# Kernel tuning notes

Measured on AMD Instinct MI355X. Metric: run time of the kernel, lower is better.

## Reference

```python
import jax, jax.numpy as jnp
import numpy as np

N_HEADS = 16

def setup_inputs() -> dict:
    key = jax.random.key(0)
    k1, k2, k3 = jax.random.split(key, 3)
    B, T, C = 4, 2048, 1024
    x = jax.random.normal(k1, (B, T, C), dtype=jnp.float32)
    w_qkv = jax.random.normal(k2, (C, 3 * C), dtype=jnp.float32) * (1.0 / np.sqrt(C))
    w_out = jax.random.normal(k3, (C, C), dtype=jnp.float32) * (1.0 / np.sqrt(C))
    return {"x": x, "w_qkv": w_qkv, "w_out": w_out}

def reference(x, w_qkv, w_out):
    B, T, C = x.shape
    H = N_HEADS
    D = C // H
    qkv = jnp.einsum('btc,cf->btf', x, w_qkv).reshape(B, T, 3, H, D)
    q, k, v = qkv[:, :, 0], qkv[:, :, 1], qkv[:, :, 2]  # [B,T,H,D]
    q = q.transpose(0, 2, 1, 3)  # [B,H,T,D]
    k = k.transpose(0, 2, 1, 3)
    v = v.transpose(0, 2, 1, 3)
    scale = 1.0 / jnp.sqrt(jnp.asarray(D, dtype=x.dtype))
    scores = jnp.einsum('bhqd,bhkd->bhqk', q, k) * scale  # [B,H,T,T]
    causal = jnp.tril(jnp.ones((T, T), dtype=bool))
    scores = jnp.where(causal[None, None], scores, jnp.asarray(-jnp.inf, dtype=scores.dtype))
    attn = jax.nn.softmax(scores, axis=-1)
    ctx = jnp.einsum('bhqk,bhkd->bhqd', attn, v)  # [B,H,T,D]
    ctx = ctx.transpose(0, 2, 1, 3).reshape(B, T, C)
    return jnp.einsum('btc,co->bto', ctx, w_out)
```

## Files before the change

kernel.cpp:

```cpp
#include <hip/hip_runtime.h>

typedef __attribute__((ext_vector_type(8))) short bf16x8;
typedef __attribute__((ext_vector_type(4))) short bf16x4;
typedef __attribute__((ext_vector_type(4))) float f32x4;
typedef __attribute__((ext_vector_type(4))) unsigned short u16x4;

#define MFMA16(a, b, c) __builtin_amdgcn_mfma_f32_16x16x32_bf16((a), (b), (c), 0, 0, 0)
#define MFMA16K16(a, b, c) __builtin_amdgcn_mfma_f32_16x16x16bf16_1k((a), (b), (c), 0, 0, 0)

__device__ __forceinline__ unsigned short f2bf(float f) {
    union { float f; unsigned int u; } x; x.f = f;
    unsigned int r = x.u + 0x7FFFu + ((x.u >> 16) & 1u);
    return (unsigned short)(r >> 16);
}
__device__ __forceinline__ unsigned int fbits(float f) {
    union { float f; unsigned int u; } x; x.f = f;
    return x.u;
}
__device__ __forceinline__ void gload_lds16(const void* g, void* l) {
    __builtin_amdgcn_global_load_lds(
        (const __attribute__((address_space(1))) unsigned int*)g,
        (__attribute__((address_space(3))) unsigned int*)l,
        16, 0, 0);
}

__global__ void cast_x(const float* __restrict__ in, unsigned short* __restrict__ hi,
                       int n) {
    int i = (blockIdx.x * blockDim.x + threadIdx.x) * 4;
    if (i >= n) return;
    float4 v = *(const float4*)(in + i);
    float vv[4] = {v.x, v.y, v.z, v.w};
    u16x4 h;
#pragma unroll
    for (int j = 0; j < 4; ++j) h[j] = f2bf(vv[j]);
    *(u16x4*)(hi + i) = h;
}

__global__ void tcast_k(const float* __restrict__ in, unsigned short* __restrict__ out,
                        int K, int N) {
    __shared__ float tile[64][65];
    int n0 = blockIdx.x * 64, k0 = blockIdx.y * 64;
    for (int i = threadIdx.x; i < 4096; i += 256) {
        int r = i >> 6, c = i & 63;
        tile[r][c] = in[(size_t)(k0 + r) * N + n0 + c];
    }
    __syncthreads();
    for (int i = threadIdx.x; i < 4096; i += 256) {
        int r = i >> 6, c = i & 63;
        out[(size_t)(n0 + r) * K + k0 + c] = f2bf(tile[c][r]);
    }
}

__global__ __launch_bounds__(256, 2) void gemm_qkv(
    const unsigned short* __restrict__ A,
    const unsigned short* __restrict__ Bt,
    unsigned short* __restrict__ qout, unsigned short* __restrict__ kout,
    unsigned short* __restrict__ vtout) {
    const int K = 1024;
    __shared__ __align__(16) unsigned short sA[128 * 64], sB[128 * 64];
    int tid = threadIdx.x, lane = tid & 63, w = tid >> 6;
    int c = lane & 15, quad = lane >> 4;
    int sw = c & 7;
    int wm = (w >> 1) * 64, wn = (w & 1) * 64;
    int m0 = blockIdx.y * 128, n0 = blockIdx.x * 128;

    f32x4 acc[4][4];
#pragma unroll
    for (int i = 0; i < 4; i++)
#pragma unroll
        for (int j = 0; j < 4; j++) acc[i][j] = (f32x4){0.f, 0.f, 0.f, 0.f};

    for (int kk = 0; kk < K; kk += 64) {
#pragma unroll
        for (int p = 0; p < 4; ++p) {
            int ch = p * 256 + tid;
            int r = ch >> 3;
            int gs = (ch & 7) ^ (r & 7);
            gload_lds16(A + (size_t)(m0 + r) * K + kk + gs * 8, &sA[ch * 8]);
            gload_lds16(Bt + (size_t)(n0 + r) * K + kk + gs * 8, &sB[ch * 8]);
        }
        __syncthreads();
#pragma unroll
        for (int ks8 = 0; ks8 < 8; ks8 += 4) {
            bf16x8 af[4], bfr[4];
#pragma unroll
            for (int mt = 0; mt < 4; ++mt)
                af[mt] = *(const bf16x8*)&sA[(wm + mt * 16 + c) * 64 +
                                             ((ks8 + quad) ^ sw) * 8];
#pragma unroll
            for (int nt = 0; nt < 4; ++nt)
                bfr[nt] = *(const bf16x8*)&sB[(wn + nt * 16 + c) * 64 +
                                              ((ks8 + quad) ^ sw) * 8];
#pragma unroll
            for (int mt = 0; mt < 4; ++mt)
#pragma unroll
                for (int nt = 0; nt < 4; ++nt)
                    acc[mt][nt] = MFMA16(af[mt], bfr[nt], acc[mt][nt]);
        }
        __syncthreads();
    }

    const float QSCALE = 0.1803368801111601f;
#pragma unroll
    for (int mt = 0; mt < 4; ++mt) {
#pragma unroll
        for (int nt = 0; nt < 4; ++nt) {
#pragma unroll
            for (int r = 0; r < 4; ++r) {
                int row = m0 + wm + mt * 16 + quad * 4 + r;
                int col = n0 + wn + nt * 16 + c;
                float v = acc[mt][nt][r];
                int which = col >> 10;
                int h = (col >> 6) & 15;
                int d = col & 63;
                int b = row >> 11;
                int t = row & 2047;
                size_t bh_ = (size_t)(b * 16 + h);
                if (which == 0)
                    qout[(bh_ * 2048 + t) * 64 + d] = f2bf(v * QSCALE);
                else if (which == 1)
                    kout[(bh_ * 2048 + t) * 64 + d] = f2bf(v);
                else
                    vtout[(bh_ * 64 + d) * 2048 + t] = f2bf(v);
            }
        }
    }
}

__global__ __launch_bounds__(256, 2) void gemm2_bt(
    const unsigned short* __restrict__ A,
    const unsigned short* __restrict__ Bt,
    float* __restrict__ out) {
    const int K = 1024, N = 1024;
    __shared__ __align__(16) unsigned short sA[128 * 64], sB[128 * 64];
    int tid = threadIdx.x, lane = tid & 63, w = tid >> 6;
    int c = lane & 15, quad = lane >> 4;
    int sw = c & 7;
    int wm = (w >> 1) * 64, wn = (w & 1) * 64;
    int m0 = blockIdx.y * 128, n0 = blockIdx.x * 128;

    f32x4 acc[4][4];
#pragma unroll
    for (int i = 0; i < 4; i++)
#pragma unroll
        for (int j = 0; j < 4; j++) acc[i][j] = (f32x4){0.f, 0.f, 0.f, 0.f};

    for (int kk = 0; kk < K; kk += 64) {
#pragma unroll
        for (int p = 0; p < 4; ++p) {
            int ch = p * 256 + tid;
            int r = ch >> 3;
            int gs = (ch & 7) ^ (r & 7);
            gload_lds16(A + (size_t)(m0 + r) * K + kk + gs * 8, &sA[ch * 8]);
            gload_lds16(Bt + (size_t)(n0 + r) * K + kk + gs * 8, &sB[ch * 8]);
        }
        __syncthreads();
#pragma unroll
        for (int ks8 = 0; ks8 < 8; ks8 += 4) {
            bf16x8 af[4], bfr[4];
#pragma unroll
            for (int mt = 0; mt < 4; ++mt)
                af[mt] = *(const bf16x8*)&sA[(wm + mt * 16 + c) * 64 +
                                             ((ks8 + quad) ^ sw) * 8];
#pragma unroll
            for (int nt = 0; nt < 4; ++nt)
                bfr[nt] = *(const bf16x8*)&sB[(wn + nt * 16 + c) * 64 +
                                              ((ks8 + quad) ^ sw) * 8];
#pragma unroll
            for (int mt = 0; mt < 4; ++mt)
#pragma unroll
                for (int nt = 0; nt < 4; ++nt)
                    acc[mt][nt] = MFMA16(af[mt], bfr[nt], acc[mt][nt]);
        }
        __syncthreads();
    }

#pragma unroll
    for (int mt = 0; mt < 4; ++mt)
#pragma unroll
        for (int nt = 0; nt < 4; ++nt)
#pragma unroll
            for (int r = 0; r < 4; ++r) {
                int row = m0 + wm + mt * 16 + quad * 4 + r;
                int col = n0 + wn + nt * 16 + c;
                out[(size_t)row * N + col] = acc[mt][nt][r];
            }
}

#define SSTR 72
__global__ __launch_bounds__(256, 4) void attn_k(
    const unsigned short* __restrict__ q,
    const unsigned short* __restrict__ k,
    const unsigned short* __restrict__ vt,
    unsigned short* __restrict__ ctx) {
    const int T = 2048, D = 64;
    __shared__ __align__(16) unsigned short sK[2][64 * SSTR];
    __shared__ __align__(16) unsigned short sV[2][64 * SSTR];

    int tid = threadIdx.x, lane = tid & 63, w = tid >> 6;
    int c = lane & 15, quad = lane >> 4;

    int j = blockIdx.x;
    int g4 = j >> 8, q4 = (j >> 4) & 15, low = j & 15;
    int jt = (g4 & 1) ? q4 : (15 - q4);
    int bh = g4 * 16 + low;
    int b = bh >> 4, hh = bh & 15;

    const unsigned short* qh = q + (size_t)bh * T * D;
    const unsigned short* kh = k + (size_t)bh * T * D;
    const unsigned short* vh = vt + (size_t)bh * D * T;

    int dv = tid >> 3, tcv = (tid & 7) * 8;
    int q0 = jt * 128;
    int nkt = 2 * jt + 2;
    int qloc = w * 16 + c;
    int qrow[2];
    qrow[0] = q0 + qloc;
    qrow[1] = qrow[0] + 64;

    bf16x8 bq[2][2];
#pragma unroll
    for (int g = 0; g < 2; ++g) {
        bq[g][0] = *(const bf16x8*)&qh[(size_t)qrow[g] * D + quad * 8];
        bq[g][1] = *(const bf16x8*)&qh[(size_t)qrow[g] * D + 32 + quad * 8];
    }

    f32x4 o[2][4];
#pragma unroll
    for (int g = 0; g < 2; ++g)
#pragma unroll
        for (int nt = 0; nt < 4; ++nt) o[g][nt] = (f32x4){0.f, 0.f, 0.f, 0.f};
    float l_i[2] = {0.f, 0.f};

    bf16x8 kr0 = *(const bf16x8*)&kh[(size_t)lane * D + w * 8];
    bf16x8 kr1 = *(const bf16x8*)&kh[(size_t)lane * D + w * 8 + 32];
    bf16x8 vr0 = *(const bf16x8*)&vh[(size_t)dv * T + tcv];
    bf16x8 vr1 = *(const bf16x8*)&vh[(size_t)(dv + 32) * T + tcv];
    *(bf16x8*)&sK[0][lane * SSTR + w * 8] = kr0;
    *(bf16x8*)&sK[0][lane * SSTR + w * 8 + 32] = kr1;
    *(bf16x8*)&sV[0][dv * SSTR + tcv] = vr0;
    *(bf16x8*)&sV[0][(dv + 32) * SSTR + tcv] = vr1;
    __syncthreads();

    int cur = 0;
    for (int kt = 0; kt < nkt; ++kt) {
        int kb = kt * 64;
        if (kt + 1 < nkt) {
            int kb2 = kb + 64;
            kr0 = *(const bf16x8*)&kh[(size_t)(kb2 + lane) * D + w * 8];
            kr1 = *(const bf16x8*)&kh[(size_t)(kb2 + lane) * D + w * 8 + 32];
            vr0 = *(const bf16x8*)&vh[(size_t)dv * T + kb2 + tcv];
            vr1 = *(const bf16x8*)&vh[(size_t)(dv + 32) * T + kb2 + tcv];
        }
        bool g0_active = (kt + 1 < nkt);

        const unsigned short* sKc = sK[cur];
        const unsigned short* sVc = sV[cur];

        f32x4 st[2][4];
        __builtin_amdgcn_s_setprio(1);
#pragma unroll
        for (int mt = 0; mt < 4; ++mt) {
            bf16x8 ak0 = *(const bf16x8*)&sKc[(mt * 16 + c) * SSTR + quad * 8];
            bf16x8 ak1 = *(const bf16x8*)&sKc[(mt * 16 + c) * SSTR + 32 + quad * 8];
#pragma unroll
            for (int g = 0; g < 2; ++g) {
                f32x4 z = (f32x4){0.f, 0.f, 0.f, 0.f};
                z = MFMA16(ak0, bq[g][0], z);
                z = MFMA16(ak1, bq[g][1], z);
                st[g][mt] = z;
            }
        }
        __builtin_amdgcn_s_setprio(0);

        bf16x4 pf[2][4];
#pragma unroll
        for (int g = 0; g < 2; ++g) {
            if (g == 0 && !g0_active) continue;
            bool diag = (kb == q0 + (g << 6));
            if (diag) {
#pragma unroll
                for (int mt = 0; mt < 4; ++mt)
#pragma unroll
                    for (int r = 0; r < 4; ++r)
                        if (mt * 16 + quad * 4 + r > qloc) st[g][mt][r] = -1.0e30f;
            }
            float rs = 0.f;
#pragma unroll
            for (int mt = 0; mt < 4; ++mt) {
                float p0 = __builtin_exp2f(st[g][mt][0]);
                float p1 = __builtin_exp2f(st[g][mt][1]);
                float p2 = __builtin_exp2f(st[g][mt][2]);
                float p3 = __builtin_exp2f(st[g][mt][3]);
                rs += (p0 + p1) + (p2 + p3);
                unsigned int w0 = __builtin_amdgcn_perm(
                    fbits(p1) + 0x8000u, fbits(p0) + 0x8000u, 0x07060302u);
                unsigned int w1 = __builtin_amdgcn_perm(
                    fbits(p3) + 0x8000u, fbits(p2) + 0x8000u, 0x07060302u);
                uint2 pk; pk.x = w0; pk.y = w1;
                pf[g][mt] = *(bf16x4*)&pk;
            }
            l_i[g] += rs;
        }

        __builtin_amdgcn_s_setprio(1);
#pragma unroll
        for (int mt = 0; mt < 4; ++mt) {
#pragma unroll
            for (int nt = 0; nt < 4; ++nt) {
                bf16x4 av = *(const bf16x4*)&sVc[(nt * 16 + c) * SSTR + mt * 16 + quad * 4];
                if (g0_active) o[0][nt] = MFMA16K16(av, pf[0][mt], o[0][nt]);
                o[1][nt] = MFMA16K16(av, pf[1][mt], o[1][nt]);
            }
        }
        __builtin_amdgcn_s_setprio(0);

        if (kt + 1 < nkt) {
            int nxt = cur ^ 1;
            *(bf16x8*)&sK[nxt][lane * SSTR + w * 8] = kr0;
            *(bf16x8*)&sK[nxt][lane * SSTR + w * 8 + 32] = kr1;
            *(bf16x8*)&sV[nxt][dv * SSTR + tcv] = vr0;
            *(bf16x8*)&sV[nxt][(dv + 32) * SSTR + tcv] = vr1;
            __syncthreads();
            cur = nxt;
        }
    }

#pragma unroll
    for (int g = 0; g < 2; ++g) {
        float l = l_i[g];
        l += __shfl_xor(l, 16);
        l += __shfl_xor(l, 32);
        float inv = 1.0f / l;
#pragma unroll
        for (int nt = 0; nt < 4; ++nt) {
            u16x4 ob;
#pragma unroll
            for (int r = 0; r < 4; ++r) ob[r] = f2bf(o[g][nt][r] * inv);
            *(u16x4*)&ctx[(size_t)(b * T + qrow[g]) * 1024 + hh * 64 + nt * 16 + quad * 4] = ob;
        }
    }
}

extern "C" void kernel_launch(void* const* d_in, const int* in_sizes, int n_in,
                              void* d_out, int out_size, void* d_ws, size_t ws_size,
                              hipStream_t stream) {
    const float* x     = (const float*)d_in[0];
    const float* w_qkv = (const float*)d_in[1];
    const float* w_out = (const float*)d_in[2];
    float* out = (float*)d_out;

    char* ws = (char*)d_ws;
    unsigned short* wqkvt = (unsigned short*)(ws + 0);
    unsigned short* woutt = (unsigned short*)(ws + 6291456);
    unsigned short* x_bf  = (unsigned short*)(ws + 8388608);
    unsigned short* qb    = (unsigned short*)(ws + 25165824);
    unsigned short* kb    = (unsigned short*)(ws + 41943040);
    unsigned short* vtb   = (unsigned short*)(ws + 58720256);
    unsigned short* ctx   = (unsigned short*)(ws + 8388608);

    cast_x<<<8192, 256, 0, stream>>>(x, x_bf, 8388608);
    tcast_k<<<dim3(48, 16), 256, 0, stream>>>(w_qkv, wqkvt, 1024, 3072);
    tcast_k<<<dim3(16, 16), 256, 0, stream>>>(w_out, woutt, 1024, 1024);
    gemm_qkv<<<dim3(24, 64), 256, 0, stream>>>(x_bf, wqkvt, qb, kb, vtb);
    attn_k<<<1024, 256, 0, stream>>>(qb, kb, vtb, ctx);
    gemm2_bt<<<dim3(8, 64), 256, 0, stream>>>(ctx, woutt, out);
}
```

Before: 266.7 us.

## Split long causal attention rows into two KV halves with atomic merge

Query tiles with long causal KV ranges (jt 8-15) are split into two blocks, each covering half of the KV tiles. Each half accumulates unnormalized partial outputs and row sums into a scratch buffer with float atomics, and a new merge kernel normalizes the result and writes ctx. The output buffer is reused as scratch and zeroed inside the cast kernel. Blocks are issued in a longest-first job order to balance load. The goal is to shorten the tail of the causal workload, at the cost of atomic traffic and an extra kernel launch. The merge is valid only because the softmax skips the max-subtraction.

```diff
diff --git a/kernel.cpp b/kernel.cpp
--- a/kernel.cpp
+++ b/kernel.cpp
@@ -25,15 +25,18 @@
 }
 
 __global__ void cast_x(const float* __restrict__ in, unsigned short* __restrict__ hi,
-                       int n) {
-    int i = (blockIdx.x * blockDim.x + threadIdx.x) * 4;
-    if (i >= n) return;
-    float4 v = *(const float4*)(in + i);
-    float vv[4] = {v.x, v.y, v.z, v.w};
-    u16x4 h;
-#pragma unroll
-    for (int j = 0; j < 4; ++j) h[j] = f2bf(vv[j]);
-    *(u16x4*)(hi + i) = h;
+                       int n, float4* __restrict__ zptr, int zn) {
+    int idx = blockIdx.x * blockDim.x + threadIdx.x;
+    int i = idx * 4;
+    if (i < n) {
+        float4 v = *(const float4*)(in + i);
+        float vv[4] = {v.x, v.y, v.z, v.w};
+        u16x4 h;
+#pragma unroll
+        for (int j = 0; j < 4; ++j) h[j] = f2bf(vv[j]);
+        *(u16x4*)(hi + i) = h;
+    }
+    if (idx < zn) zptr[idx] = (float4){0.f, 0.f, 0.f, 0.f};
 }
 
 __global__ void tcast_k(const float* __restrict__ in, unsigned short* __restrict__ out,
@@ -188,11 +191,15 @@
 }
 
 #define SSTR 72
+__device__ const int JOB_ORDER[24] = {7, 15, 23, 14, 22, 6,  13, 21, 12, 20, 5,  11,
+                                      19, 10, 18, 4,  9,  17, 8,  16, 3,  2,  1,  0};
+
 __global__ __launch_bounds__(256, 4) void attn_k(
     const unsigned short* __restrict__ q,
     const unsigned short* __restrict__ k,
     const unsigned short* __restrict__ vt,
-    unsigned short* __restrict__ ctx) {
+    unsigned short* __restrict__ ctx,
+    float* __restrict__ op, float* __restrict__ lbuf) {
     const int T = 2048, D = 64;
     __shared__ __align__(16) unsigned short sK[2][64 * SSTR];
     __shared__ __align__(16) unsigned short sV[2][64 * SSTR];
@@ -200,10 +207,14 @@
     int tid = threadIdx.x, lane = tid & 63, w = tid >> 6;
     int c = lane & 15, quad = lane >> 4;
 
-    int j = blockIdx.x;
-    int g4 = j >> 8, q4 = (j >> 4) & 15, low = j & 15;
-    int jt = (g4 & 1) ? q4 : (15 - q4);
-    int bh = g4 * 16 + low;
+    int rank = blockIdx.x >> 6, bh = blockIdx.x & 63;
+    int t = JOB_ORDER[rank];
+    int jt, kt0, nkt;
+    bool split, has_diag;
+    if (t < 8)        { jt = t;     kt0 = 0;      nkt = 2 * t + 2; split = false; has_diag = true; }
+    else if (t < 16)  { jt = t;     kt0 = 0;      nkt = jt + 1;    split = true;  has_diag = false; }
+    else              { jt = t - 8; kt0 = jt + 1; nkt = jt + 1;    split = true;  has_diag = true; }
+    int kt_end = kt0 + nkt;
     int b = bh >> 4, hh = bh & 15;
 
     const unsigned short* qh = q + (size_t)bh * T * D;
@@ -212,7 +223,6 @@
 
     int dv = tid >> 3, tcv = (tid & 7) * 8;
     int q0 = jt * 128;
-    int nkt = 2 * jt + 2;
     int qloc = w * 16 + c;
     int qrow[2];
     qrow[0] = q0 + qloc;
@@ -232,10 +242,11 @@
         for (int nt = 0; nt < 4; ++nt) o[g][nt] = (f32x4){0.f, 0.f, 0.f, 0.f};
     float l_i[2] = {0.f, 0.f};
 
-    bf16x8 kr0 = *(const bf16x8*)&kh[(size_t)lane * D + w * 8];
-    bf16x8 kr1 = *(const bf16x8*)&kh[(size_t)lane * D + w * 8 + 32];
-    bf16x8 vr0 = *(const bf16x8*)&vh[(size_t)dv * T + tcv];
-    bf16x8 vr1 = *(const bf16x8*)&vh[(size_t)(dv + 32) * T + tcv];
+    int kb0 = kt0 * 64;
+    bf16x8 kr0 = *(const bf16x8*)&kh[(size_t)(kb0 + lane) * D + w * 8];
+    bf16x8 kr1 = *(const bf16x8*)&kh[(size_t)(kb0 + lane) * D + w * 8 + 32];
+    bf16x8 vr0 = *(const bf16x8*)&vh[(size_t)dv * T + kb0 + tcv];
+    bf16x8 vr1 = *(const bf16x8*)&vh[(size_t)(dv + 32) * T + kb0 + tcv];
     *(bf16x8*)&sK[0][lane * SSTR + w * 8] = kr0;
     *(bf16x8*)&sK[0][lane * SSTR + w * 8 + 32] = kr1;
     *(bf16x8*)&sV[0][dv * SSTR + tcv] = vr0;
@@ -243,16 +254,16 @@
     __syncthreads();
 
     int cur = 0;
-    for (int kt = 0; kt < nkt; ++kt) {
+    for (int kt = kt0; kt < kt_end; ++kt) {
         int kb = kt * 64;
-        if (kt + 1 < nkt) {
+        if (kt + 1 < kt_end) {
             int kb2 = kb + 64;
             kr0 = *(const bf16x8*)&kh[(size_t)(kb2 + lane) * D + w * 8];
             kr1 = *(const bf16x8*)&kh[(size_t)(kb2 + lane) * D + w * 8 + 32];
             vr0 = *(const bf16x8*)&vh[(size_t)dv * T + kb2 + tcv];
             vr1 = *(const bf16x8*)&vh[(size_t)(dv + 32) * T + kb2 + tcv];
         }
-        bool g0_active = (kt + 1 < nkt);
+        bool g0_active = !has_diag || (kt != 2 * jt + 1);
 
         const unsigned short* sKc = sK[cur];
         const unsigned short* sVc = sV[cur];
@@ -277,7 +288,7 @@
 #pragma unroll
         for (int g = 0; g < 2; ++g) {
             if (g == 0 && !g0_active) continue;
-            bool diag = (kb == q0 + (g << 6));
+            bool diag = has_diag && (kb == q0 + (g << 6));
             if (diag) {
 #pragma unroll
                 for (int mt = 0; mt < 4; ++mt)
@@ -315,7 +326,7 @@
         }
         __builtin_amdgcn_s_setprio(0);
 
-        if (kt + 1 < nkt) {
+        if (kt + 1 < kt_end) {
             int nxt = cur ^ 1;
             *(bf16x8*)&sK[nxt][lane * SSTR + w * 8] = kr0;
             *(bf16x8*)&sK[nxt][lane * SSTR + w * 8 + 32] = kr1;
@@ -326,20 +337,56 @@
         }
     }
 
-#pragma unroll
-    for (int g = 0; g < 2; ++g) {
-        float l = l_i[g];
-        l += __shfl_xor(l, 16);
-        l += __shfl_xor(l, 32);
-        float inv = 1.0f / l;
-#pragma unroll
-        for (int nt = 0; nt < 4; ++nt) {
-            u16x4 ob;
-#pragma unroll
-            for (int r = 0; r < 4; ++r) ob[r] = f2bf(o[g][nt][r] * inv);
-            *(u16x4*)&ctx[(size_t)(b * T + qrow[g]) * 1024 + hh * 64 + nt * 16 + quad * 4] = ob;
-        }
-    }
+    if (!split) {
+#pragma unroll
+        for (int g = 0; g < 2; ++g) {
+            float l = l_i[g];
+            l += __shfl_xor(l, 16);
+            l += __shfl_xor(l, 32);
+            float inv = 1.0f / l;
+#pragma unroll
+            for (int nt = 0; nt < 4; ++nt) {
+                u16x4 ob;
+#pragma unroll
+                for (int r = 0; r < 4; ++r) ob[r] = f2bf(o[g][nt][r] * inv);
+                *(u16x4*)&ctx[(size_t)(b * T + qrow[g]) * 1024 + hh * 64 + nt * 16 + quad * 4] = ob;
+            }
+        }
+    } else {
+        int sidx = bh * 8 + (jt - 8);
+#pragma unroll
+        for (int g = 0; g < 2; ++g) {
+            float l = l_i[g];
+            l += __shfl_xor(l, 16);
+            l += __shfl_xor(l, 32);
+            int rloc = qrow[g] - q0;
+            if (quad == 0) atomicAdd(&lbuf[sidx * 128 + rloc], l);
+            float* orow = op + ((size_t)sidx * 128 + rloc) * 64;
+#pragma unroll
+            for (int nt = 0; nt < 4; ++nt)
+#pragma unroll
+                for (int r = 0; r < 4; ++r)
+                    atomicAdd(&orow[nt * 16 + quad * 4 + r], o[g][nt][r]);
+        }
+    }
+}
+
+__global__ void merge_k(const float* __restrict__ op, const float* __restrict__ lbuf,
+                        unsigned short* __restrict__ ctx) {
+    int gid = blockIdx.x * 256 + threadIdx.x;
+    int row = gid >> 4, dq = (gid & 15) * 4;
+    int sidx = row >> 7, rloc = row & 127;
+    int bh = sidx >> 3, jt = 8 + (sidx & 7);
+    int b = bh >> 4, hh = bh & 15;
+    int tq = jt * 128 + rloc;
+    float inv = 1.0f / lbuf[row];
+    float4 o = *(const float4*)(op + (size_t)row * 64 + dq);
+    u16x4 ob;
+    ob[0] = f2bf(o.x * inv);
+    ob[1] = f2bf(o.y * inv);
+    ob[2] = f2bf(o.z * inv);
+    ob[3] = f2bf(o.w * inv);
+    *(u16x4*)&ctx[((size_t)(b * 2048 + tq)) * 1024 + hh * 64 + dq] = ob;
 }
 
 extern "C" void kernel_launch(void* const* d_in, const int* in_sizes, int n_in,
@@ -359,10 +406,14 @@
     unsigned short* vtb   = (unsigned short*)(ws + 58720256);
     unsigned short* ctx   = (unsigned short*)(ws + 8388608);
 
-    cast_x<<<8192, 256, 0, stream>>>(x, x_bf, 8388608);
+    float* op   = (float*)d_out;
+    float* lbuf = (float*)((char*)d_out + 16777216);
+
+    cast_x<<<8192, 256, 0, stream>>>(x, x_bf, 8388608, (float4*)d_out, 1064960);
     tcast_k<<<dim3(48, 16), 256, 0, stream>>>(w_qkv, wqkvt, 1024, 3072);
     tcast_k<<<dim3(16, 16), 256, 0, stream>>>(w_out, woutt, 1024, 1024);
     gemm_qkv<<<dim3(24, 64), 256, 0, stream>>>(x_bf, wqkvt, qb, kb, vtb);
-    attn_k<<<1024, 256, 0, stream>>>(qb, kb, vtb, ctx);
+    attn_k<<<1536, 256, 0, stream>>>(qb, kb, vtb, ctx, op, lbuf);
+    merge_k<<<4096, 256, 0, stream>>>(op, lbuf, ctx);
     gemm2_bt<<<dim3(8, 64), 256, 0, stream>>>(ctx, woutt, out);
 }
```

Measured after the change: 360.7 us. 35.2% more time.
